# Kernel tuning notes

Measured on AMD Instinct MI355X. Metric: run time of the kernel, lower is better.

## Reference

```python
import jax, jax.numpy as jnp
import numpy as np

LN_EPS = 1e-5      # torch nn.LayerNorm default
NORM_EPS = 1e-12   # torch F.normalize default


def _layer_norm(x, gamma, beta):
    mu = jnp.mean(x, axis=-1, keepdims=True)
    var = jnp.mean((x - mu) ** 2, axis=-1, keepdims=True)
    return (x - mu) * jax.lax.rsqrt(var + LN_EPS) * gamma + beta


def _l2_normalize_rows(w):
    n = jnp.sqrt(jnp.sum(w * w, axis=1, keepdims=True))
    return w / jnp.maximum(n, NORM_EPS)


def setup_inputs() -> dict:
    key = jax.random.key(0)
    B, D = 32768, 512
    ks = jax.random.split(key, 4)
    return {
        "stimulus": jax.random.normal(ks[0], (B, D), dtype=jnp.float32),
        "prev_activation": jax.random.normal(ks[1], (B, D), dtype=jnp.float32),
        "W": jax.random.normal(ks[2], (D, D), dtype=jnp.float32),
        "Wr": jax.random.normal(ks[3], (D, D), dtype=jnp.float32),
        "alpha": jnp.full((D,), 0.1, dtype=jnp.float32),
        "decay": jnp.full((D,), 0.01, dtype=jnp.float32),
        "ln_act_gamma": jnp.ones((D,), dtype=jnp.float32),
        "ln_act_beta": jnp.zeros((D,), dtype=jnp.float32),
        "ln_rec_gamma": jnp.ones((D,), dtype=jnp.float32),
        "ln_rec_beta": jnp.zeros((D,), dtype=jnp.float32),
    }


def reference(stimulus, prev_activation, W, Wr, alpha, decay,
              ln_act_gamma, ln_act_beta, ln_rec_gamma, ln_rec_beta):
    # recurrent path
    rec_out = prev_activation @ Wr                      # [B, D]
    rec_norm = _layer_norm(rec_out, ln_rec_gamma, ln_rec_beta)
    # stimulus path
    stim_out = stimulus @ W                             # [B, D]
    final = jax.nn.relu(stim_out + rec_norm)
    final = _layer_norm(final, ln_act_gamma, ln_act_beta)

    # Hebbian weight update (detached in the original module)
    heb_upd = jnp.einsum('bi,bj->ij', stimulus, stim_out) * alpha[None, :]
    rec_upd = jnp.einsum('bi,bj->ij', prev_activation, rec_out) * alpha[None, :]
    # diag(decay) @ W is a row-wise broadcast scale
    new_W = _l2_normalize_rows(W + heb_upd - decay[:, None] * W)
    new_Wr = _l2_normalize_rows(Wr + rec_upd - decay[:, None] * Wr)

    return final, new_W, new_Wr
```

## Files before the change

kernel.cpp:

```cpp
#include <hip/hip_runtime.h>
#include <stdint.h>

typedef unsigned int u32;
typedef unsigned short u16;
typedef float  f32x4 __attribute__((ext_vector_type(4)));
typedef u32    u32x4 __attribute__((ext_vector_type(4)));
typedef __bf16 bf16x8 __attribute__((ext_vector_type(8)));

static __device__ __forceinline__ u16 f2bf(float f){
  u32 u = __builtin_bit_cast(u32, f);
  return (u16)((u + 0x7FFFu + ((u >> 16) & 1u)) >> 16);
}

static __device__ __forceinline__ void async16(const void* g, void* l){
  __builtin_amdgcn_global_load_lds((const __attribute__((address_space(1))) u32*)g,
                                   (__attribute__((address_space(3))) u32*)l, 16, 0, 0);
}

static __device__ __forceinline__ float wave_sum(float v){
#pragma unroll
  for (int o = 32; o > 0; o >>= 1) v += __shfl_xor(v, o, 64);
  return v;
}

__global__ __launch_bounds__(256) void k_tcvt(const float* __restrict__ s0, const float* __restrict__ s1,
                                              u16* __restrict__ d0, u16* __restrict__ d1,
                                              int R, int C){
  const float* __restrict__ src = blockIdx.z ? s1 : s0;
  u16* __restrict__ dst = blockIdx.z ? d1 : d0;
  __shared__ u16 lt[64*72];
  const int c0 = blockIdx.x * 64, r0 = blockIdx.y * 64;
  const int tid = threadIdx.x;
  const int rr = tid >> 4, c4 = tid & 15;
#pragma unroll
  for (int p = 0; p < 4; ++p){
    int r = rr + p*16;
    f32x4 f = *(const f32x4*)(src + (size_t)(r0 + r)*C + c0 + c4*4);
#pragma unroll
    for (int e = 0; e < 4; ++e) lt[(c4*4 + e)*72 + r] = f2bf(f[e]);
  }
  __syncthreads();
  const int c = tid >> 2, bg = tid & 3;
  const u32x4* lp = (const u32x4*)(lt + c*72 + bg*16);
  u32x4 w0 = lp[0], w1 = lp[1];
  u16* drow = dst + (size_t)(c0 + c)*R + r0 + bg*16;
  *(u32x4*)drow = w0;
  *(u32x4*)(drow + 8) = w1;
}

__global__ __launch_bounds__(256) void k_gemm_fwd(const float* __restrict__ A,
                                                  const u16* __restrict__ Bt,
                                                  u16* __restrict__ Cn,
                                                  u16* __restrict__ Ct){
  __shared__ char smem[49152];
  float* sA = (float*)smem;
  u16*   sB = (u16*)(smem + 32768);
  const int tid = threadIdx.x;
  const int lane = tid & 63, wid = tid >> 6;
  const int wm = wid >> 1, wn = wid & 1;
  const int l15 = lane & 15, q = lane >> 4;
  const int id = blockIdx.x;
  const int c8 = id & 7, g = id >> 3;
  const int yb = c8*32 + (g >> 2), xb = g & 3;
  const int m0 = yb * 128, n0 = xb * 128;

  f32x4 acc[4][4];
  const f32x4 vzero = {0.f, 0.f, 0.f, 0.f};
#pragma unroll
  for (int a = 0; a < 4; ++a)
#pragma unroll
    for (int b = 0; b < 4; ++b) acc[a][b] = vzero;

#pragma unroll 1
  for (int kt = 0; kt < 8; ++kt){
    const int k0 = kt*64;
#pragma unroll
    for (int it = 0; it < 8; ++it){
      int gg0 = it*256 + tid;
      int r = gg0 >> 4, gp = gg0 & 15;
      int gsw = gp ^ (r & 15);
      async16(A + (size_t)(m0 + r)*512 + k0 + gsw*4, (char*)sA + (size_t)gg0*16);
    }
#pragma unroll
    for (int it = 0; it < 4; ++it){
      int gg0 = it*256 + tid;
      int r = gg0 >> 3, gp = gg0 & 7;
      int gsw = gp ^ (r & 7);
      async16(Bt + (size_t)(n0 + r)*512 + k0 + gsw*8, (char*)sB + (size_t)gg0*16);
    }
    __syncthreads();
#pragma unroll
    for (int kk = 0; kk < 2; ++kk){
      bf16x8 af[4], bfv[4];
#pragma unroll
      for (int mt = 0; mt < 4; ++mt){
        int r = wm*64 + mt*16 + l15;
        int d0i = (kk*8 + q*2) ^ (r & 15);
        int d1i = (kk*8 + q*2 + 1) ^ (r & 15);
        f32x4 f0 = *(const f32x4*)(sA + (size_t)(r*16 + d0i)*4);
        f32x4 f1 = *(const f32x4*)(sA + (size_t)(r*16 + d1i)*4);
        bf16x8 a;
        a[0]=(__bf16)f0[0]; a[1]=(__bf16)f0[1]; a[2]=(__bf16)f0[2]; a[3]=(__bf16)f0[3];
        a[4]=(__bf16)f1[0]; a[5]=(__bf16)f1[1]; a[6]=(__bf16)f1[2]; a[7]=(__bf16)f1[3];
        af[mt] = a;
      }
#pragma unroll
      for (int nt = 0; nt < 4; ++nt){
        int r = wn*64 + nt*16 + l15;
        int gsw = (kk*4 + q) ^ (r & 7);
        bfv[nt] = *(const bf16x8*)(sB + (size_t)(r*8 + gsw)*8);
      }
#pragma unroll
      for (int mt = 0; mt < 4; ++mt)
#pragma unroll
        for (int nt = 0; nt < 4; ++nt)
          acc[mt][nt] = __builtin_amdgcn_mfma_f32_16x16x32_bf16(af[mt], bfv[nt], acc[mt][nt], 0, 0, 0);
    }
    __syncthreads();
  }

  u16* lt = (u16*)smem;
#pragma unroll
  for (int mt = 0; mt < 4; ++mt)
#pragma unroll
    for (int nt = 0; nt < 4; ++nt){
      f32x4 v = acc[mt][nt];
      u16 b0 = f2bf(v[0]), b1 = f2bf(v[1]), b2 = f2bf(v[2]), b3 = f2bf(v[3]);
      int n = wn*64 + nt*16 + l15;
      int mb = wm*64 + mt*16 + q*4;
      u16* cn = Cn + (size_t)(m0 + mb)*512 + n0 + n;
      cn[0] = b0; cn[512] = b1; cn[1024] = b2; cn[1536] = b3;
      *(u32*)(lt + n*136 + mb)     = (u32)b0 | ((u32)b1 << 16);
      *(u32*)(lt + n*136 + mb + 2) = (u32)b2 | ((u32)b3 << 16);
    }
  __syncthreads();
#pragma unroll
  for (int p = 0; p < 8; ++p){
    int gg0 = p*256 + tid;
    int n = gg0 >> 4, mg = gg0 & 15;
    u32x4 w = *(const u32x4*)(lt + n*136 + mg*8);
    *(u32x4*)(Ct + (size_t)(n0 + n)*32768 + m0 + mg*8) = w;
  }
}

__global__ __launch_bounds__(256) void k_gemm_upd(const u16* __restrict__ A0, const u16* __restrict__ B0,
                                                  const u16* __restrict__ A1, const u16* __restrict__ B1,
                                                  float* __restrict__ part){
  __shared__ char smem[32768];
  u16* sA = (u16*)smem;
  u16* sB = (u16*)(smem + 16384);
  const int tid = threadIdx.x;
  const int lane = tid & 63, wid = tid >> 6;
  const int wm = wid >> 1, wn = wid & 1;
  const int l15 = lane & 15, q = lane >> 4;
  const int id = blockIdx.x;
  const int c8 = id & 7, g = id >> 3;
  const int zz = c8*8 + (g >> 4);
  const int xb = g & 3, yb = (g >> 2) & 3;
  const int mat = zz >> 5, sp = zz & 31;
  const u16* __restrict__ A = mat ? A1 : A0;
  const u16* __restrict__ B = mat ? B1 : B0;
  const int m0 = yb * 128, n0 = xb * 128;
  const int kb = sp * 1024;

  f32x4 acc[4][4];
  const f32x4 vzero = {0.f, 0.f, 0.f, 0.f};
#pragma unroll
  for (int a = 0; a < 4; ++a)
#pragma unroll
    for (int b = 0; b < 4; ++b) acc[a][b] = vzero;

#pragma unroll 1
  for (int kt = 0; kt < 16; ++kt){
    const int k0 = kb + kt*64;
#pragma unroll
    for (int it = 0; it < 4; ++it){
      int gg0 = it*256 + tid;
      int r = gg0 >> 3, gp = gg0 & 7, gsw = gp ^ (r & 7);
      async16(A + (size_t)(m0 + r)*32768 + k0 + gsw*8, (char*)sA + (size_t)gg0*16);
    }
#pragma unroll
    for (int it = 0; it < 4; ++it){
      int gg0 = it*256 + tid;
      int r = gg0 >> 3, gp = gg0 & 7, gsw = gp ^ (r & 7);
      async16(B + (size_t)(n0 + r)*32768 + k0 + gsw*8, (char*)sB + (size_t)gg0*16);
    }
    __syncthreads();
#pragma unroll
    for (int kk = 0; kk < 2; ++kk){
      bf16x8 af[4], bfv[4];
#pragma unroll
      for (int mt = 0; mt < 4; ++mt){
        int r = wm*64 + mt*16 + l15;
        int gsw = (kk*4 + q) ^ (r & 7);
        af[mt] = *(const bf16x8*)(sA + (size_t)(r*8 + gsw)*8);
      }
#pragma unroll
      for (int nt = 0; nt < 4; ++nt){
        int r = wn*64 + nt*16 + l15;
        int gsw = (kk*4 + q) ^ (r & 7);
        bfv[nt] = *(const bf16x8*)(sB + (size_t)(r*8 + gsw)*8);
      }
#pragma unroll
      for (int mt = 0; mt < 4; ++mt)
#pragma unroll
        for (int nt = 0; nt < 4; ++nt)
          acc[mt][nt] = __builtin_amdgcn_mfma_f32_16x16x32_bf16(af[mt], bfv[nt], acc[mt][nt], 0, 0, 0);
    }
    __syncthreads();
  }

  float* dst = part + (size_t)(mat*32 + sp)*262144;
#pragma unroll
  for (int mt = 0; mt < 4; ++mt)
#pragma unroll
    for (int nt = 0; nt < 4; ++nt){
      f32x4 v = acc[mt][nt];
      int n = wn*64 + nt*16 + l15;
      int mb = wm*64 + mt*16 + q*4;
      float* d = dst + (size_t)(m0 + mb)*512 + n0 + n;
      d[0] = v[0]; d[512] = v[1]; d[1024] = v[2]; d[1536] = v[3];
    }
}

__global__ __launch_bounds__(256) void k_ln(const u16* __restrict__ SO, const u16* __restrict__ RO,
                                            const float* __restrict__ ga, const float* __restrict__ ba,
                                            const float* __restrict__ gr, const float* __restrict__ br,
                                            float* __restrict__ out){
  const int wid = threadIdx.x >> 6, lane = threadIdx.x & 63;
  const size_t b = (size_t)blockIdx.x*4 + wid;
  const int c = lane*8;
  float x[8], t[8];
  {
    u32x4 u = *(const u32x4*)(RO + b*512 + c);
#pragma unroll
    for (int i = 0; i < 4; ++i){
      u32 w = u[i];
      x[2*i]   = __uint_as_float(w << 16);
      x[2*i+1] = __uint_as_float(w & 0xFFFF0000u);
    }
  }
  float s = 0.f, ss = 0.f;
#pragma unroll
  for (int e = 0; e < 8; ++e){ s += x[e]; ss += x[e]*x[e]; }
  s = wave_sum(s); ss = wave_sum(ss);
  float mu = s*(1.f/512.f);
  float var = fmaxf(ss*(1.f/512.f) - mu*mu, 0.f);
  float rs = rsqrtf(var + 1e-5f);
  f32x4 g0 = *(const f32x4*)(gr + c), g1 = *(const f32x4*)(gr + c + 4);
  f32x4 h0 = *(const f32x4*)(br + c), h1 = *(const f32x4*)(br + c + 4);
  {
    u32x4 u = *(const u32x4*)(SO + b*512 + c);
    float so[8];
#pragma unroll
    for (int i = 0; i < 4; ++i){
      u32 w = u[i];
      so[2*i]   = __uint_as_float(w << 16);
      so[2*i+1] = __uint_as_float(w & 0xFFFF0000u);
    }
#pragma unroll
    for (int e = 0; e < 4; ++e) t[e]   = fmaxf(so[e]   + (x[e]  -mu)*rs*g0[e] + h0[e], 0.f);
#pragma unroll
    for (int e = 0; e < 4; ++e) t[4+e] = fmaxf(so[4+e] + (x[4+e]-mu)*rs*g1[e] + h1[e], 0.f);
  }
  float s2 = 0.f, ss2 = 0.f;
#pragma unroll
  for (int e = 0; e < 8; ++e){ s2 += t[e]; ss2 += t[e]*t[e]; }
  s2 = wave_sum(s2); ss2 = wave_sum(ss2);
  float mu2 = s2*(1.f/512.f);
  float var2 = fmaxf(ss2*(1.f/512.f) - mu2*mu2, 0.f);
  float rs2 = rsqrtf(var2 + 1e-5f);
  f32x4 G0 = *(const f32x4*)(ga + c), G1 = *(const f32x4*)(ga + c + 4);
  f32x4 H0 = *(const f32x4*)(ba + c), H1 = *(const f32x4*)(ba + c + 4);
  f32x4 o0, o1;
#pragma unroll
  for (int e = 0; e < 4; ++e){
    o0[e] = (t[e]   - mu2)*rs2*G0[e] + H0[e];
    o1[e] = (t[4+e] - mu2)*rs2*G1[e] + H1[e];
  }
  *(f32x4*)(out + b*512 + c)     = o0;
  *(f32x4*)(out + b*512 + c + 4) = o1;
}

__global__ __launch_bounds__(256) void k_finalize(const float* __restrict__ W0, const float* __restrict__ W1,
                                                  const float* __restrict__ part,
                                                  const float* __restrict__ alpha, const float* __restrict__ decay,
                                                  float* __restrict__ out){
  const int i = blockIdx.x, mat = blockIdx.y;
  const int t = threadIdx.x;
  const float* Wm = mat ? W1 : W0;
  const float* pb = part + (size_t)mat*32*262144 + (size_t)i*512;
  const float dc = decay[i];
  float v[2], ssq = 0.f;
#pragma unroll
  for (int h = 0; h < 2; ++h){
    int j = t + h*256;
    float acc = 0.f;
#pragma unroll
    for (int sp = 0; sp < 32; ++sp) acc += pb[(size_t)sp*262144 + j];
    float val = Wm[(size_t)i*512 + j]*(1.f - dc) + alpha[j]*acc;
    v[h] = val; ssq += val*val;
  }
  float wsum = wave_sum(ssq);
  __shared__ float red[4];
  const int lane = t & 63, wid = t >> 6;
  if (lane == 0) red[wid] = wsum;
  __syncthreads();
  float tot = red[0] + red[1] + red[2] + red[3];
  float rn = 1.f / fmaxf(sqrtf(tot), 1e-12f);
  out[(size_t)mat*262144 + (size_t)i*512 + t]       = v[0]*rn;
  out[(size_t)mat*262144 + (size_t)i*512 + t + 256] = v[1]*rn;
}

extern "C" void kernel_launch(void* const* d_in, const int* in_sizes, int n_in,
                              void* d_out, int out_size, void* d_ws, size_t ws_size,
                              hipStream_t stream) {
  const float* S  = (const float*)d_in[0];
  const float* P  = (const float*)d_in[1];
  const float* W  = (const float*)d_in[2];
  const float* Wr = (const float*)d_in[3];
  const float* alpha = (const float*)d_in[4];
  const float* decay = (const float*)d_in[5];
  const float* ga = (const float*)d_in[6];
  const float* ba = (const float*)d_in[7];
  const float* gr = (const float*)d_in[8];
  const float* br = (const float*)d_in[9];
  float* out = (float*)d_out;

  char* ws = (char*)d_ws;
  u16* ST  = (u16*)(ws);
  u16* PT  = (u16*)(ws + 33554432);
  u16* SOT = (u16*)(ws + 67108864);
  u16* ROT = (u16*)(ws + 100663296);
  u16* SO  = (u16*)(ws + 134217728);
  u16* RO  = (u16*)(ws + 167772160);
  u16* Wt  = (u16*)(ws + 201326592);
  u16* Wrt = (u16*)(ws + 201850880);
  float* part = (float*)(ws + 134217728);

  dim3 blk(256);
  k_tcvt<<<dim3(8, 512, 2), blk, 0, stream>>>(S, P, ST, PT, 32768, 512);
  k_tcvt<<<dim3(8, 8, 2),   blk, 0, stream>>>(W, Wr, Wt, Wrt, 512, 512);
  k_gemm_fwd<<<dim3(1024), blk, 0, stream>>>(S, Wt,  SO, SOT);
  k_gemm_fwd<<<dim3(1024), blk, 0, stream>>>(P, Wrt, RO, ROT);
  k_ln<<<dim3(8192), blk, 0, stream>>>(SO, RO, ga, ba, gr, br, out);
  k_gemm_upd<<<dim3(1024), blk, 0, stream>>>(ST, SOT, PT, ROT, part);
  k_finalize<<<dim3(512, 2), blk, 0, stream>>>(W, Wr, part, alpha, decay, out + 16777216);
}
```

Baseline: 372.7 us.

## Replace input transpose with plain bf16 convert; transpose A tiles in LDS in update GEMM

The transposing fp32-to-bf16 conversion of the stimulus and previous-activation matrices becomes a plain row-major conversion. The update GEMM now loads row-major tiles and transposes them in shared memory before the MFMA loop. The forward GEMM reads the bf16 copies instead of converting fp32 in its inner loop, and both forward GEMMs merge into one launch with 512-thread blocks and 256-row tiles. The update GEMM also moves to 512 threads with 256-wide N tiles. This removes a strided transpose pass and halves the forward A-tile traffic, at the cost of an extra LDS transpose and barrier per K step plus higher shared-memory use per block.

```diff
diff --git a/kernel.cpp b/kernel.cpp
--- a/kernel.cpp
+++ b/kernel.cpp
@@ -21,6 +21,21 @@
 #pragma unroll
   for (int o = 32; o > 0; o >>= 1) v += __shfl_xor(v, o, 64);
   return v;
+}
+
+__global__ __launch_bounds__(256) void k_cvt(const float* __restrict__ s0, const float* __restrict__ s1,
+                                             u16* __restrict__ d0, u16* __restrict__ d1){
+  const float* __restrict__ src = blockIdx.y ? s1 : s0;
+  u16* __restrict__ dst = blockIdx.y ? d1 : d0;
+  size_t i = ((size_t)blockIdx.x*256 + threadIdx.x) * 8;
+  f32x4 a = *(const f32x4*)(src + i);
+  f32x4 b = *(const f32x4*)(src + i + 4);
+  u32x4 w;
+  w[0] = (u32)f2bf(a[0]) | ((u32)f2bf(a[1]) << 16);
+  w[1] = (u32)f2bf(a[2]) | ((u32)f2bf(a[3]) << 16);
+  w[2] = (u32)f2bf(b[0]) | ((u32)f2bf(b[1]) << 16);
+  w[3] = (u32)f2bf(b[2]) | ((u32)f2bf(b[3]) << 16);
+  *(u32x4*)(dst + i) = w;
 }
 
 __global__ __launch_bounds__(256) void k_tcvt(const float* __restrict__ s0, const float* __restrict__ s1,
@@ -48,21 +63,26 @@
   *(u32x4*)(drow + 8) = w1;
 }
 
-__global__ __launch_bounds__(256) void k_gemm_fwd(const float* __restrict__ A,
-                                                  const u16* __restrict__ Bt,
-                                                  u16* __restrict__ Cn,
-                                                  u16* __restrict__ Ct){
-  __shared__ char smem[49152];
-  float* sA = (float*)smem;
-  u16*   sB = (u16*)(smem + 32768);
+__global__ __launch_bounds__(512) void k_gemm_fwd(const u16* __restrict__ SN, const u16* __restrict__ PN,
+                                                  const u16* __restrict__ Wt, const u16* __restrict__ Wrt,
+                                                  u16* __restrict__ SO, u16* __restrict__ RO,
+                                                  u16* __restrict__ SOT, u16* __restrict__ ROT){
+  __shared__ char smem[67584];
+  u16* sA = (u16*)smem;
+  u16* sB = (u16*)(smem + 32768);
   const int tid = threadIdx.x;
   const int lane = tid & 63, wid = tid >> 6;
   const int wm = wid >> 1, wn = wid & 1;
   const int l15 = lane & 15, q = lane >> 4;
   const int id = blockIdx.x;
   const int c8 = id & 7, g = id >> 3;
-  const int yb = c8*32 + (g >> 2), xb = g & 3;
-  const int m0 = yb * 128, n0 = xb * 128;
+  const int sel = g >> 6, h = g & 63;
+  const int yb = c8*16 + (h >> 2), xb = h & 3;
+  const int m0 = yb * 256, n0 = xb * 128;
+  const u16* __restrict__ A  = sel ? PN  : SN;
+  const u16* __restrict__ Bt = sel ? Wrt : Wt;
+  u16* __restrict__ Cn = sel ? RO  : SO;
+  u16* __restrict__ Ct = sel ? ROT : SOT;
 
   f32x4 acc[4][4];
   const f32x4 vzero = {0.f, 0.f, 0.f, 0.f};
@@ -75,17 +95,15 @@
   for (int kt = 0; kt < 8; ++kt){
     const int k0 = kt*64;
 #pragma unroll
-    for (int it = 0; it < 8; ++it){
-      int gg0 = it*256 + tid;
-      int r = gg0 >> 4, gp = gg0 & 15;
-      int gsw = gp ^ (r & 15);
-      async16(A + (size_t)(m0 + r)*512 + k0 + gsw*4, (char*)sA + (size_t)gg0*16);
-    }
-#pragma unroll
     for (int it = 0; it < 4; ++it){
-      int gg0 = it*256 + tid;
-      int r = gg0 >> 3, gp = gg0 & 7;
-      int gsw = gp ^ (r & 7);
+      int gg0 = it*512 + tid;
+      int r = gg0 >> 3, gp = gg0 & 7, gsw = gp ^ (r & 7);
+      async16(A + (size_t)(m0 + r)*512 + k0 + gsw*8, (char*)sA + (size_t)gg0*16);
+    }
+#pragma unroll
+    for (int it = 0; it < 2; ++it){
+      int gg0 = it*512 + tid;
+      int r = gg0 >> 3, gp = gg0 & 7, gsw = gp ^ (r & 7);
       async16(Bt + (size_t)(n0 + r)*512 + k0 + gsw*8, (char*)sB + (size_t)gg0*16);
     }
     __syncthreads();
@@ -95,14 +113,8 @@
 #pragma unroll
       for (int mt = 0; mt < 4; ++mt){
         int r = wm*64 + mt*16 + l15;
-        int d0i = (kk*8 + q*2) ^ (r & 15);
-        int d1i = (kk*8 + q*2 + 1) ^ (r & 15);
-        f32x4 f0 = *(const f32x4*)(sA + (size_t)(r*16 + d0i)*4);
-        f32x4 f1 = *(const f32x4*)(sA + (size_t)(r*16 + d1i)*4);
-        bf16x8 a;
-        a[0]=(__bf16)f0[0]; a[1]=(__bf16)f0[1]; a[2]=(__bf16)f0[2]; a[3]=(__bf16)f0[3];
-        a[4]=(__bf16)f1[0]; a[5]=(__bf16)f1[1]; a[6]=(__bf16)f1[2]; a[7]=(__bf16)f1[3];
-        af[mt] = a;
+        int gsw = (kk*4 + q) ^ (r & 7);
+        af[mt] = *(const bf16x8*)(sA + (size_t)(r*8 + gsw)*8);
       }
 #pragma unroll
       for (int nt = 0; nt < 4; ++nt){
@@ -130,38 +142,42 @@
       int mb = wm*64 + mt*16 + q*4;
       u16* cn = Cn + (size_t)(m0 + mb)*512 + n0 + n;
       cn[0] = b0; cn[512] = b1; cn[1024] = b2; cn[1536] = b3;
-      *(u32*)(lt + n*136 + mb)     = (u32)b0 | ((u32)b1 << 16);
-      *(u32*)(lt + n*136 + mb + 2) = (u32)b2 | ((u32)b3 << 16);
+      *(u32*)(lt + n*264 + mb)     = (u32)b0 | ((u32)b1 << 16);
+      *(u32*)(lt + n*264 + mb + 2) = (u32)b2 | ((u32)b3 << 16);
     }
   __syncthreads();
 #pragma unroll
   for (int p = 0; p < 8; ++p){
-    int gg0 = p*256 + tid;
-    int n = gg0 >> 4, mg = gg0 & 15;
-    u32x4 w = *(const u32x4*)(lt + n*136 + mg*8);
+    int gg0 = p*512 + tid;
+    int n = gg0 >> 5, mg = gg0 & 31;
+    u32x4 w = *(const u32x4*)(lt + n*264 + mg*8);
     *(u32x4*)(Ct + (size_t)(n0 + n)*32768 + m0 + mg*8) = w;
   }
 }
 
-__global__ __launch_bounds__(256) void k_gemm_upd(const u16* __restrict__ A0, const u16* __restrict__ B0,
+__global__ __launch_bounds__(512) void k_gemm_upd(const u16* __restrict__ A0, const u16* __restrict__ B0,
                                                   const u16* __restrict__ A1, const u16* __restrict__ B1,
                                                   float* __restrict__ part){
-  __shared__ char smem[32768];
-  u16* sA = (u16*)smem;
-  u16* sB = (u16*)(smem + 16384);
+  __shared__ char smem[67584];
+  char* sAn = smem;
+  u32*  sAt = (u32*)(smem + 16384);
+  u16*  sB  = (u16*)(smem + 34816);
   const int tid = threadIdx.x;
   const int lane = tid & 63, wid = tid >> 6;
-  const int wm = wid >> 1, wn = wid & 1;
+  const int wm = wid >> 2, wn = wid & 3;
   const int l15 = lane & 15, q = lane >> 4;
   const int id = blockIdx.x;
   const int c8 = id & 7, g = id >> 3;
-  const int zz = c8*8 + (g >> 4);
-  const int xb = g & 3, yb = (g >> 2) & 3;
+  const int zz = c8*8 + (g >> 3);
+  const int xy = g & 7;
   const int mat = zz >> 5, sp = zz & 31;
+  const int yb = xy & 3, xb = xy >> 2;
   const u16* __restrict__ A = mat ? A1 : A0;
   const u16* __restrict__ B = mat ? B1 : B0;
-  const int m0 = yb * 128, n0 = xb * 128;
+  const int m0 = yb * 128, n0 = xb * 256;
   const int kb = sp * 1024;
+  const int base_c = tid >> 5, pr = tid & 31;
+  const int ce = (base_c + pr) & 15;
 
   f32x4 acc[4][4];
   const f32x4 vzero = {0.f, 0.f, 0.f, 0.f};
@@ -174,26 +190,36 @@
   for (int kt = 0; kt < 16; ++kt){
     const int k0 = kb + kt*64;
 #pragma unroll
+    for (int it = 0; it < 2; ++it){
+      int gg0 = it*512 + tid;
+      int r = gg0 >> 4, gp = gg0 & 15;
+      async16(A + (size_t)(k0 + r)*512 + m0 + gp*8, sAn + (size_t)gg0*16);
+    }
+#pragma unroll
     for (int it = 0; it < 4; ++it){
-      int gg0 = it*256 + tid;
-      int r = gg0 >> 3, gp = gg0 & 7, gsw = gp ^ (r & 7);
-      async16(A + (size_t)(m0 + r)*32768 + k0 + gsw*8, (char*)sA + (size_t)gg0*16);
-    }
-#pragma unroll
-    for (int it = 0; it < 4; ++it){
-      int gg0 = it*256 + tid;
+      int gg0 = it*512 + tid;
       int r = gg0 >> 3, gp = gg0 & 7, gsw = gp ^ (r & 7);
       async16(B + (size_t)(n0 + r)*32768 + k0 + gsw*8, (char*)sB + (size_t)gg0*16);
     }
     __syncthreads();
+    {
+      u32x4 r0 = *(const u32x4*)(sAn + (size_t)(2*pr)*256 + ce*16);
+      u32x4 r1 = *(const u32x4*)(sAn + (size_t)(2*pr)*256 + 256 + ce*16);
+#pragma unroll
+      for (int e = 0; e < 4; ++e){
+        u32 lo = r0[e], hi = r1[e];
+        sAt[(ce*8 + 2*e    )*36 + pr] = (lo & 0xFFFFu) | (hi << 16);
+        sAt[(ce*8 + 2*e + 1)*36 + pr] = (lo >> 16) | (hi & 0xFFFF0000u);
+      }
+    }
+    __syncthreads();
 #pragma unroll
     for (int kk = 0; kk < 2; ++kk){
       bf16x8 af[4], bfv[4];
 #pragma unroll
       for (int mt = 0; mt < 4; ++mt){
         int r = wm*64 + mt*16 + l15;
-        int gsw = (kk*4 + q) ^ (r & 7);
-        af[mt] = *(const bf16x8*)(sA + (size_t)(r*8 + gsw)*8);
+        af[mt] = *(const bf16x8*)(sAt + (size_t)r*36 + kk*16 + q*4);
       }
 #pragma unroll
       for (int nt = 0; nt < 4; ++nt){
@@ -328,8 +354,8 @@
   float* out = (float*)d_out;
 
   char* ws = (char*)d_ws;
-  u16* ST  = (u16*)(ws);
-  u16* PT  = (u16*)(ws + 33554432);
+  u16* SN  = (u16*)(ws);
+  u16* PN  = (u16*)(ws + 33554432);
   u16* SOT = (u16*)(ws + 67108864);
   u16* ROT = (u16*)(ws + 100663296);
   u16* SO  = (u16*)(ws + 134217728);
@@ -338,12 +364,10 @@
   u16* Wrt = (u16*)(ws + 201850880);
   float* part = (float*)(ws + 134217728);
 
-  dim3 blk(256);
-  k_tcvt<<<dim3(8, 512, 2), blk, 0, stream>>>(S, P, ST, PT, 32768, 512);
-  k_tcvt<<<dim3(8, 8, 2),   blk, 0, stream>>>(W, Wr, Wt, Wrt, 512, 512);
-  k_gemm_fwd<<<dim3(1024), blk, 0, stream>>>(S, Wt,  SO, SOT);
-  k_gemm_fwd<<<dim3(1024), blk, 0, stream>>>(P, Wrt, RO, ROT);
-  k_ln<<<dim3(8192), blk, 0, stream>>>(SO, RO, ga, ba, gr, br, out);
-  k_gemm_upd<<<dim3(1024), blk, 0, stream>>>(ST, SOT, PT, ROT, part);
-  k_finalize<<<dim3(512, 2), blk, 0, stream>>>(W, Wr, part, alpha, decay, out + 16777216);
-}
+  k_cvt<<<dim3(8192, 2), dim3(256), 0, stream>>>(S, P, SN, PN);
+  k_tcvt<<<dim3(8, 8, 2), dim3(256), 0, stream>>>(W, Wr, Wt, Wrt, 512, 512);
+  k_gemm_fwd<<<dim3(1024), dim3(512), 0, stream>>>(SN, PN, Wt, Wrt, SO, RO, SOT, ROT);
+  k_ln<<<dim3(8192), dim3(256), 0, stream>>>(SO, RO, ga, ba, gr, br, out);
+  k_gemm_upd<<<dim3(512), dim3(512), 0, stream>>>(SN, SOT, PN, ROT, part);
+  k_finalize<<<dim3(512, 2), dim3(256), 0, stream>>>(W, Wr, part, alpha, decay, out + 16777216);
+}
```

After: 324.1 us. 1.15x faster.
